# Performance work log

Measured on AMD Instinct MI355X. Metric: run time of the kernel, lower is better.

The kernel has to match this reference:

```python
import jax, jax.numpy as jnp
import numpy as np


def setup_inputs() -> dict:
    key = jax.random.key(0)
    k1, k2 = jax.random.split(key)
    B, C, H = 1024, 1000, 512  # batch, classes, hidden
    y = jax.random.normal(k1, (B, C), dtype=jnp.float32)
    w = jax.random.normal(k2, (C, H), dtype=jnp.float32)
    epsilon = jnp.ones((), dtype=jnp.float32)
    lipschitz = jnp.ones((), dtype=jnp.float32)
    return {"y": y, "w": w, "epsilon": epsilon, "lipschitz": lipschitz}


def reference(y, w, epsilon, lipschitz):
    # y: [B, C] logits; w: [C, H] final-layer weight
    kW = lipschitz * w.T                      # [H, C]
    j = jnp.argmax(y, axis=1)                 # [B]
    y_j = jnp.max(y, axis=1, keepdims=True)   # [B, 1]
    kW_j = kW.T[j]                            # [B, H] gather of argmax column
    kW_ij = kW_j[:, :, None] - kW[None]       # [B, H, C] broadcast difference
    sq = jnp.sum(kW_ij * kW_ij, axis=1)       # [B, C]
    # safe sqrt (value identical; avoids NaN grad at the exact-zero j column)
    K_ij = jnp.where(sq > 0, jnp.sqrt(jnp.where(sq > 0, sq, 1.0)), 0.0)
    y_bot_i = y + epsilon * K_ij              # [B, C]
    y_bot_i = jnp.where(y == y_j, -jnp.inf, y_bot_i)
    y_bot = jnp.max(y_bot_i, axis=1, keepdims=True)  # [B, 1]
    return jnp.concatenate([y, y_bot], axis=1)       # [B, C+1]
```

## Files before the change

### kernel.cpp

```cpp
#include <hip/hip_runtime.h>
#include <math.h>

#define B_SZ 1024
#define C_SZ 1000
#define H_SZ 512


typedef __attribute__((ext_vector_type(8))) short bf16x8;
typedef __attribute__((ext_vector_type(4))) float f32x4;

__global__ __launch_bounds__(256) void k_prep(
    const float* __restrict__ y, const float* __restrict__ w,
    int* __restrict__ jv, float* __restrict__ ymax,
    float* __restrict__ wnorm, short* __restrict__ wbf,
    float* __restrict__ out) {
    const int r = blockIdx.x;
    const int tid = threadIdx.x;
    if (r < 250) {
        const int wave = tid >> 6, lane = tid & 63;
        const int c = r * 4 + wave;
        const float* row = w + c * H_SZ;
        float4 a = *(const float4*)(row + lane * 8);
        float4 b = *(const float4*)(row + lane * 8 + 4);
        float f[8] = {a.x, a.y, a.z, a.w, b.x, b.y, b.z, b.w};
        unsigned short u[8];
        float s = 0.f;
#pragma unroll
        for (int i = 0; i < 8; ++i) {
            s += f[i] * f[i];
            unsigned v = __float_as_uint(f[i]);
            v += 0x7fffu + ((v >> 16) & 1u);
            u[i] = (unsigned short)(v >> 16);
        }
        uint4 pk;
        pk.x = (unsigned)u[0] | ((unsigned)u[1] << 16);
        pk.y = (unsigned)u[2] | ((unsigned)u[3] << 16);
        pk.z = (unsigned)u[4] | ((unsigned)u[5] << 16);
        pk.w = (unsigned)u[6] | ((unsigned)u[7] << 16);
        *(uint4*)(wbf + c * H_SZ + lane * 8) = pk;
#pragma unroll
        for (int off = 32; off; off >>= 1) s += __shfl_down(s, off, 64);
        if (lane == 0) wnorm[c] = s;
    } else {
        const int b = r - 250;
        const float* yrow = y + b * C_SZ;
        float* orow = out + b * (C_SZ + 1);
        float best = -INFINITY;
        int bidx = 0x7fffffff;
        if (tid < 250) {
            float4 v = *(const float4*)(yrow + tid * 4);
            float e[4] = {v.x, v.y, v.z, v.w};
#pragma unroll
            for (int i = 0; i < 4; ++i) {
                orow[tid * 4 + i] = e[i];
                if (e[i] > best) { best = e[i]; bidx = tid * 4 + i; }
            }
        }
        const int lane = tid & 63;
#pragma unroll
        for (int off = 32; off; off >>= 1) {
            float ov = __shfl_down(best, off, 64);
            int oi = __shfl_down(bidx, off, 64);
            if (ov > best || (ov == best && oi < bidx)) { best = ov; bidx = oi; }
        }
        __shared__ float sv[4];
        __shared__ int si[4];
        if (lane == 0) { sv[tid >> 6] = best; si[tid >> 6] = bidx; }
        __syncthreads();
        if (tid == 0) {
            float bv = sv[0]; int bi = si[0];
#pragma unroll
            for (int k = 1; k < 4; ++k) {
                if (sv[k] > bv || (sv[k] == bv && si[k] < bi)) { bv = sv[k]; bi = si[k]; }
            }
            jv[b] = bi;
            ymax[b] = bv;
        }
    }
}

#define KC 128
#define RS 136
__global__ __launch_bounds__(256) void k_main(
    const float* __restrict__ y, const short* __restrict__ wbf,
    const float* __restrict__ eps_p, const float* __restrict__ lip_p,
    const int* __restrict__ jv, const float* __restrict__ ymax,
    const float* __restrict__ wnorm, float* __restrict__ part) {
    __shared__ __align__(16) short As[64 * RS];
    __shared__ __align__(16) short Bs[64 * RS];
    __shared__ int sjv[64];
    __shared__ float snj[64];
    __shared__ float sym[64];

    const int t = threadIdx.x;
    const int bx = blockIdx.x, by = blockIdx.y;
    const int b0 = by * 64, c0 = bx * 64;

    if (t < 64) {
        int j = jv[b0 + t];
        sjv[t] = j;
        snj[t] = wnorm[j];
        sym[t] = ymax[b0 + t];
    }
    __syncthreads();

    const int srow = t >> 2;
    const int sseg = t & 3;
    int crow = c0 + srow; if (crow > C_SZ - 1) crow = C_SZ - 1;
    const short* agsrc = wbf + sjv[srow] * H_SZ;
    const short* bgsrc = wbf + crow * H_SZ;

    uint4 pa[4], pb[4];
#pragma unroll
    for (int p = 0; p < 4; ++p) {
        const int off = (sseg + p * 4) * 8;
        pa[p] = *(const uint4*)(agsrc + off);
        pb[p] = *(const uint4*)(bgsrc + off);
    }

    const int wv = t >> 6, lane = t & 63;
    const int col = lane & 15, quad = lane >> 4;
    const short* ard = &As[(wv * 16 + col) * RS + quad * 8];
    const short* brd = &Bs[col * RS + quad * 8];

    f32x4 acc[4] = {{0.f, 0.f, 0.f, 0.f},
                    {0.f, 0.f, 0.f, 0.f},
                    {0.f, 0.f, 0.f, 0.f},
                    {0.f, 0.f, 0.f, 0.f}};

    for (int ch = 0; ch < 4; ++ch) {
#pragma unroll
        for (int p = 0; p < 4; ++p) {
            const int off = (sseg + p * 4) * 8;
            *(uint4*)&As[srow * RS + off] = pa[p];
            *(uint4*)&Bs[srow * RS + off] = pb[p];
        }
        __syncthreads();
        if (ch < 3) {
            const int gbase = (ch + 1) * KC;
#pragma unroll
            for (int p = 0; p < 4; ++p) {
                const int off = gbase + (sseg + p * 4) * 8;
                pa[p] = *(const uint4*)(agsrc + off);
                pb[p] = *(const uint4*)(bgsrc + off);
            }
        }
#pragma unroll
        for (int ks = 0; ks < 4; ++ks) {
            bf16x8 af = *(const bf16x8*)(ard + ks * 32);
#pragma unroll
            for (int ct = 0; ct < 4; ++ct) {
                bf16x8 bf = *(const bf16x8*)(brd + ct * 16 * RS + ks * 32);
                acc[ct] =
                    __builtin_amdgcn_mfma_f32_16x16x32_bf16(af, bf, acc[ct], 0, 0, 0);
            }
        }
        __syncthreads();
    }

    const float eps = *eps_p;
    const float L = *lip_p;
    const float L2 = L * L;
    float rmax[4];
#pragma unroll
    for (int i = 0; i < 4; ++i) {
        const int br = wv * 16 + quad * 4 + i;
        const int b = b0 + br;
        const float nj = snj[br];
        const float ym = sym[br];
        float m = -INFINITY;
#pragma unroll
        for (int ct = 0; ct < 4; ++ct) {
            const int cc = c0 + ct * 16 + col;
            if (cc < C_SZ) {
                const float yv = y[b * C_SZ + cc];
                const float nc = wnorm[cc];
                const float sq = L2 * (nj + nc - 2.0f * acc[ct][i]);
                const float K = sq > 0.f ? sqrtf(sq) : 0.f;
                const float cand = (yv == ym) ? -INFINITY : yv + eps * K;
                m = fmaxf(m, cand);
            }
        }
        rmax[i] = m;
    }
#pragma unroll
    for (int off = 8; off; off >>= 1)
#pragma unroll
        for (int i = 0; i < 4; ++i)
            rmax[i] = fmaxf(rmax[i], __shfl_xor(rmax[i], off, 64));
    if (col == 0) {
        float* slice = part + bx * B_SZ;
#pragma unroll
        for (int i = 0; i < 4; ++i)
            slice[b0 + wv * 16 + quad * 4 + i] = rmax[i];
    }
}

__global__ void k_final(const float* __restrict__ part,
                        float* __restrict__ out) {
    int b = blockIdx.x * 256 + threadIdx.x;
    if (b >= B_SZ) return;
    float m = -INFINITY;
#pragma unroll
    for (int s = 0; s < 16; ++s) m = fmaxf(m, part[s * B_SZ + b]);
    out[b * (C_SZ + 1) + C_SZ] = m;
}

extern "C" void kernel_launch(void* const* d_in, const int* in_sizes, int n_in,
                              void* d_out, int out_size, void* d_ws,
                              size_t ws_size, hipStream_t stream) {
    const float* y = (const float*)d_in[0];
    const float* w = (const float*)d_in[1];
    const float* eps = (const float*)d_in[2];
    const float* lip = (const float*)d_in[3];
    float* out = (float*)d_out;

    char* ws = (char*)d_ws;
    int* jv = (int*)ws;
    float* ymax = (float*)(ws + 4096);
    float* wnorm = (float*)(ws + 8192);
    float* part = (float*)(ws + 16384);
    short* wbf = (short*)(ws + 524288);

    k_prep<<<250 + B_SZ, 256, 0, stream>>>(y, w, jv, ymax, wnorm, wbf, out);
    k_main<<<dim3(16, 16), 256, 0, stream>>>(y, wbf, eps, lip, jv, ymax, wnorm,
                                             part);
    k_final<<<(B_SZ + 255) / 256, 256, 0, stream>>>(part, out);
}
```

Baseline: 82.66 us.

## Fuse prep, main and final kernels into one cooperative kernel with grid syncs

Merges the three kernels into a single cooperative launch of 256 blocks. Each block handles weight conversion for some rows, does a per-wave argmax over four y rows, grid-syncs, runs the bf16 MFMA tile, grid-syncs again, and then reduces the partial maxima. The aim is to drop two launch gaps and the separate tiny final kernel. In exchange it adds grid-wide barrier overhead, and the prep phase now runs on fewer blocks with more work per wave.

Measured after the change: 138.0 us. 1.67x slower.

```diff
diff --git a/kernel.cpp b/kernel.cpp
--- a/kernel.cpp
+++ b/kernel.cpp
@@ -1,5 +1,8 @@
 #include <hip/hip_runtime.h>
+#include <hip/hip_cooperative_groups.h>
 #include <math.h>
+
+namespace cg = cooperative_groups;
 
 #define B_SZ 1024
 #define C_SZ 1000
@@ -9,16 +12,28 @@
 typedef __attribute__((ext_vector_type(8))) short bf16x8;
 typedef __attribute__((ext_vector_type(4))) float f32x4;
 
-__global__ __launch_bounds__(256) void k_prep(
+#define KC 128
+#define RS 136
+
+__global__ __launch_bounds__(256) void k_fused(
     const float* __restrict__ y, const float* __restrict__ w,
+    const float* __restrict__ eps_p, const float* __restrict__ lip_p,
     int* __restrict__ jv, float* __restrict__ ymax,
     float* __restrict__ wnorm, short* __restrict__ wbf,
-    float* __restrict__ out) {
+    float* __restrict__ part, float* __restrict__ out) {
+    __shared__ __align__(16) short As[64 * RS];
+    __shared__ __align__(16) short Bs[64 * RS];
+    __shared__ int sjv[64];
+    __shared__ float snj[64];
+    __shared__ float sym[64];
+
+    cg::grid_group grid = cg::this_grid();
     const int r = blockIdx.x;
-    const int tid = threadIdx.x;
+    const int t = threadIdx.x;
+    const int wv = t >> 6, lane = t & 63;
+
     if (r < 250) {
-        const int wave = tid >> 6, lane = tid & 63;
-        const int c = r * 4 + wave;
+        const int c = r * 4 + wv;
         const float* row = w + c * H_SZ;
         float4 a = *(const float4*)(row + lane * 8);
         float4 b = *(const float4*)(row + lane * 8 + 4);
@@ -41,59 +56,42 @@
 #pragma unroll
         for (int off = 32; off; off >>= 1) s += __shfl_down(s, off, 64);
         if (lane == 0) wnorm[c] = s;
-    } else {
-        const int b = r - 250;
+    }
+
+    {
+        const int b = r * 4 + wv;
         const float* yrow = y + b * C_SZ;
         float* orow = out + b * (C_SZ + 1);
         float best = -INFINITY;
         int bidx = 0x7fffffff;
-        if (tid < 250) {
-            float4 v = *(const float4*)(yrow + tid * 4);
-            float e[4] = {v.x, v.y, v.z, v.w};
-#pragma unroll
-            for (int i = 0; i < 4; ++i) {
-                orow[tid * 4 + i] = e[i];
-                if (e[i] > best) { best = e[i]; bidx = tid * 4 + i; }
-            }
-        }
-        const int lane = tid & 63;
+#pragma unroll
+        for (int i = 0; i < 4; ++i) {
+            const int idx = i * 64 + lane;
+            if (idx < 250) {
+                float4 v = *(const float4*)(yrow + idx * 4);
+                *(float4*)(orow + idx * 4) = v;
+                float e[4] = {v.x, v.y, v.z, v.w};
+#pragma unroll
+                for (int j = 0; j < 4; ++j) {
+                    if (e[j] > best) { best = e[j]; bidx = idx * 4 + j; }
+                }
+            }
+        }
 #pragma unroll
         for (int off = 32; off; off >>= 1) {
             float ov = __shfl_down(best, off, 64);
             int oi = __shfl_down(bidx, off, 64);
             if (ov > best || (ov == best && oi < bidx)) { best = ov; bidx = oi; }
         }
-        __shared__ float sv[4];
-        __shared__ int si[4];
-        if (lane == 0) { sv[tid >> 6] = best; si[tid >> 6] = bidx; }
-        __syncthreads();
-        if (tid == 0) {
-            float bv = sv[0]; int bi = si[0];
-#pragma unroll
-            for (int k = 1; k < 4; ++k) {
-                if (sv[k] > bv || (sv[k] == bv && si[k] < bi)) { bv = sv[k]; bi = si[k]; }
-            }
-            jv[b] = bi;
-            ymax[b] = bv;
-        }
-    }
-}
-
-#define KC 128
-#define RS 136
-__global__ __launch_bounds__(256) void k_main(
-    const float* __restrict__ y, const short* __restrict__ wbf,
-    const float* __restrict__ eps_p, const float* __restrict__ lip_p,
-    const int* __restrict__ jv, const float* __restrict__ ymax,
-    const float* __restrict__ wnorm, float* __restrict__ part) {
-    __shared__ __align__(16) short As[64 * RS];
-    __shared__ __align__(16) short Bs[64 * RS];
-    __shared__ int sjv[64];
-    __shared__ float snj[64];
-    __shared__ float sym[64];
-
-    const int t = threadIdx.x;
-    const int bx = blockIdx.x, by = blockIdx.y;
+        if (lane == 0) {
+            jv[b] = bidx;
+            ymax[b] = best;
+        }
+    }
+
+    grid.sync();
+
+    const int by = r >> 4, bx = r & 15;
     const int b0 = by * 64, c0 = bx * 64;
 
     if (t < 64) {
@@ -106,7 +104,8 @@
 
     const int srow = t >> 2;
     const int sseg = t & 3;
-    int crow = c0 + srow; if (crow > C_SZ - 1) crow = C_SZ - 1;
+    int crow = c0 + srow;
+    if (crow > C_SZ - 1) crow = C_SZ - 1;
     const short* agsrc = wbf + sjv[srow] * H_SZ;
     const short* bgsrc = wbf + crow * H_SZ;
 
@@ -118,7 +117,6 @@
         pb[p] = *(const uint4*)(bgsrc + off);
     }
 
-    const int wv = t >> 6, lane = t & 63;
     const int col = lane & 15, quad = lane >> 4;
     const short* ard = &As[(wv * 16 + col) * RS + quad * 8];
     const short* brd = &Bs[col * RS + quad * 8];
@@ -151,8 +149,8 @@
 #pragma unroll
             for (int ct = 0; ct < 4; ++ct) {
                 bf16x8 bf = *(const bf16x8*)(brd + ct * 16 * RS + ks * 32);
-                acc[ct] =
-                    __builtin_amdgcn_mfma_f32_16x16x32_bf16(af, bf, acc[ct], 0, 0, 0);
+                acc[ct] = __builtin_amdgcn_mfma_f32_16x16x32_bf16(af, bf,
+                                                                  acc[ct], 0, 0, 0);
             }
         }
         __syncthreads();
@@ -194,16 +192,18 @@
         for (int i = 0; i < 4; ++i)
             slice[b0 + wv * 16 + quad * 4 + i] = rmax[i];
     }
-}
-
-__global__ void k_final(const float* __restrict__ part,
-                        float* __restrict__ out) {
-    int b = blockIdx.x * 256 + threadIdx.x;
-    if (b >= B_SZ) return;
-    float m = -INFINITY;
-#pragma unroll
-    for (int s = 0; s < 16; ++s) m = fmaxf(m, part[s * B_SZ + b]);
-    out[b * (C_SZ + 1) + C_SZ] = m;
+
+    grid.sync();
+
+    {
+        const int rr = r * 4 + wv;
+        float m = -INFINITY;
+        if (lane < 16) m = part[lane * B_SZ + rr];
+#pragma unroll
+        for (int off = 8; off; off >>= 1)
+            m = fmaxf(m, __shfl_xor(m, off, 64));
+        if (lane == 0) out[rr * (C_SZ + 1) + C_SZ] = m;
+    }
 }
 
 extern "C" void kernel_launch(void* const* d_in, const int* in_sizes, int n_in,
@@ -222,8 +222,9 @@
     float* part = (float*)(ws + 16384);
     short* wbf = (short*)(ws + 524288);
 
-    k_prep<<<250 + B_SZ, 256, 0, stream>>>(y, w, jv, ymax, wnorm, wbf, out);
-    k_main<<<dim3(16, 16), 256, 0, stream>>>(y, wbf, eps, lip, jv, ymax, wnorm,
-                                             part);
-    k_final<<<(B_SZ + 255) / 256, 256, 0, stream>>>(part, out);
+    void* args[] = {(void*)&y,    (void*)&w,    (void*)&eps,  (void*)&lip,
+                    (void*)&jv,   (void*)&ymax, (void*)&wnorm, (void*)&wbf,
+                    (void*)&part, (void*)&out};
+    hipLaunchCooperativeKernel((void*)k_fused, dim3(256), dim3(256), args, 0,
+                               stream);
 }
```

## Shrink main-kernel batch tile to 16 rows to launch more blocks

Applied to the files above, without the earlier changes.

The main kernel's batch tile drops from 64 to 16 rows per block. Each wave now handles one 16x16 output tile with a single accumulator, and the grid grows from 256 to 1024 blocks to fill more compute units on the GPU. Per-block row maxima are combined across waves through shared memory before being written out. The cost is that each 64-row class tile of weights is reloaded four times as often, and each block does less work relative to its fixed overhead.

Measured after the change: 86.28 us. 1.04x slower.

```diff
diff --git a/kernel.cpp b/kernel.cpp
--- a/kernel.cpp
+++ b/kernel.cpp
@@ -8,6 +8,9 @@
 
 typedef __attribute__((ext_vector_type(8))) short bf16x8;
 typedef __attribute__((ext_vector_type(4))) float f32x4;
+
+#define KC 128
+#define RS 136
 
 __global__ __launch_bounds__(256) void k_prep(
     const float* __restrict__ y, const float* __restrict__ w,
@@ -79,24 +82,25 @@
     }
 }
 
-#define KC 128
-#define RS 136
 __global__ __launch_bounds__(256) void k_main(
     const float* __restrict__ y, const short* __restrict__ wbf,
     const float* __restrict__ eps_p, const float* __restrict__ lip_p,
     const int* __restrict__ jv, const float* __restrict__ ymax,
     const float* __restrict__ wnorm, float* __restrict__ part) {
-    __shared__ __align__(16) short As[64 * RS];
+    __shared__ __align__(16) short As[16 * RS];
     __shared__ __align__(16) short Bs[64 * RS];
-    __shared__ int sjv[64];
-    __shared__ float snj[64];
-    __shared__ float sym[64];
+    __shared__ int sjv[16];
+    __shared__ float snj[16];
+    __shared__ float sym[16];
+    __shared__ float wred[4][16];
 
     const int t = threadIdx.x;
+    const int wv = t >> 6, lane = t & 63;
+    const int col = lane & 15, quad = lane >> 4;
     const int bx = blockIdx.x, by = blockIdx.y;
-    const int b0 = by * 64, c0 = bx * 64;
-
-    if (t < 64) {
+    const int b0 = by * 16, c0 = bx * 64;
+
+    if (t < 16) {
         int j = jv[b0 + t];
         sjv[t] = j;
         snj[t] = wnorm[j];
@@ -104,56 +108,48 @@
     }
     __syncthreads();
 
-    const int srow = t >> 2;
-    const int sseg = t & 3;
-    int crow = c0 + srow; if (crow > C_SZ - 1) crow = C_SZ - 1;
-    const short* agsrc = wbf + sjv[srow] * H_SZ;
-    const short* bgsrc = wbf + crow * H_SZ;
-
-    uint4 pa[4], pb[4];
+    const int arow = t >> 4;
+    const int aseg = t & 15;
+    const short* ag = wbf + sjv[arow] * H_SZ + aseg * 8;
+    int browv[4], bsegv[4];
+    const short* bg[4];
 #pragma unroll
     for (int p = 0; p < 4; ++p) {
-        const int off = (sseg + p * 4) * 8;
-        pa[p] = *(const uint4*)(agsrc + off);
-        pb[p] = *(const uint4*)(bgsrc + off);
-    }
-
-    const int wv = t >> 6, lane = t & 63;
-    const int col = lane & 15, quad = lane >> 4;
-    const short* ard = &As[(wv * 16 + col) * RS + quad * 8];
-    const short* brd = &Bs[col * RS + quad * 8];
-
-    f32x4 acc[4] = {{0.f, 0.f, 0.f, 0.f},
-                    {0.f, 0.f, 0.f, 0.f},
-                    {0.f, 0.f, 0.f, 0.f},
-                    {0.f, 0.f, 0.f, 0.f}};
+        const int idx = p * 256 + t;
+        browv[p] = idx >> 4;
+        bsegv[p] = idx & 15;
+        int cr = c0 + browv[p];
+        if (cr > C_SZ - 1) cr = C_SZ - 1;
+        bg[p] = wbf + cr * H_SZ + bsegv[p] * 8;
+    }
+
+    uint4 pa = *(const uint4*)ag;
+    uint4 pb[4];
+#pragma unroll
+    for (int p = 0; p < 4; ++p) pb[p] = *(const uint4*)bg[p];
+
+    const short* ard = &As[col * RS + quad * 8];
+    const short* brd = &Bs[(wv * 16 + col) * RS + quad * 8];
+
+    f32x4 acc = {0.f, 0.f, 0.f, 0.f};
 
     for (int ch = 0; ch < 4; ++ch) {
-#pragma unroll
-        for (int p = 0; p < 4; ++p) {
-            const int off = (sseg + p * 4) * 8;
-            *(uint4*)&As[srow * RS + off] = pa[p];
-            *(uint4*)&Bs[srow * RS + off] = pb[p];
-        }
+        *(uint4*)&As[arow * RS + aseg * 8] = pa;
+#pragma unroll
+        for (int p = 0; p < 4; ++p)
+            *(uint4*)&Bs[browv[p] * RS + bsegv[p] * 8] = pb[p];
         __syncthreads();
         if (ch < 3) {
-            const int gbase = (ch + 1) * KC;
-#pragma unroll
-            for (int p = 0; p < 4; ++p) {
-                const int off = gbase + (sseg + p * 4) * 8;
-                pa[p] = *(const uint4*)(agsrc + off);
-                pb[p] = *(const uint4*)(bgsrc + off);
-            }
+            const int go = (ch + 1) * KC;
+            pa = *(const uint4*)(ag + go);
+#pragma unroll
+            for (int p = 0; p < 4; ++p) pb[p] = *(const uint4*)(bg[p] + go);
         }
 #pragma unroll
         for (int ks = 0; ks < 4; ++ks) {
             bf16x8 af = *(const bf16x8*)(ard + ks * 32);
-#pragma unroll
-            for (int ct = 0; ct < 4; ++ct) {
-                bf16x8 bf = *(const bf16x8*)(brd + ct * 16 * RS + ks * 32);
-                acc[ct] =
-                    __builtin_amdgcn_mfma_f32_16x16x32_bf16(af, bf, acc[ct], 0, 0, 0);
-            }
+            bf16x8 bf = *(const bf16x8*)(brd + ks * 32);
+            acc = __builtin_amdgcn_mfma_f32_16x16x32_bf16(af, bf, acc, 0, 0, 0);
         }
         __syncthreads();
     }
@@ -161,27 +157,21 @@
     const float eps = *eps_p;
     const float L = *lip_p;
     const float L2 = L * L;
+    const int cc = c0 + wv * 16 + col;
+    const float nc = wnorm[cc < C_SZ ? cc : C_SZ - 1];
     float rmax[4];
 #pragma unroll
     for (int i = 0; i < 4; ++i) {
-        const int br = wv * 16 + quad * 4 + i;
+        const int br = quad * 4 + i;
         const int b = b0 + br;
-        const float nj = snj[br];
-        const float ym = sym[br];
-        float m = -INFINITY;
-#pragma unroll
-        for (int ct = 0; ct < 4; ++ct) {
-            const int cc = c0 + ct * 16 + col;
-            if (cc < C_SZ) {
-                const float yv = y[b * C_SZ + cc];
-                const float nc = wnorm[cc];
-                const float sq = L2 * (nj + nc - 2.0f * acc[ct][i]);
-                const float K = sq > 0.f ? sqrtf(sq) : 0.f;
-                const float cand = (yv == ym) ? -INFINITY : yv + eps * K;
-                m = fmaxf(m, cand);
-            }
-        }
-        rmax[i] = m;
+        float cand = -INFINITY;
+        if (cc < C_SZ) {
+            const float yv = y[b * C_SZ + cc];
+            const float sq = L2 * (snj[br] + nc - 2.0f * acc[i]);
+            const float K = sq > 0.f ? sqrtf(sq) : 0.f;
+            cand = (yv == sym[br]) ? -INFINITY : yv + eps * K;
+        }
+        rmax[i] = cand;
     }
 #pragma unroll
     for (int off = 8; off; off >>= 1)
@@ -189,10 +179,14 @@
         for (int i = 0; i < 4; ++i)
             rmax[i] = fmaxf(rmax[i], __shfl_xor(rmax[i], off, 64));
     if (col == 0) {
-        float* slice = part + bx * B_SZ;
-#pragma unroll
-        for (int i = 0; i < 4; ++i)
-            slice[b0 + wv * 16 + quad * 4 + i] = rmax[i];
+#pragma unroll
+        for (int i = 0; i < 4; ++i) wred[wv][quad * 4 + i] = rmax[i];
+    }
+    __syncthreads();
+    if (t < 16) {
+        float m = fmaxf(fmaxf(wred[0][t], wred[1][t]),
+                        fmaxf(wred[2][t], wred[3][t]));
+        part[bx * B_SZ + b0 + t] = m;
     }
 }
 
@@ -223,7 +217,7 @@
     short* wbf = (short*)(ws + 524288);
 
     k_prep<<<250 + B_SZ, 256, 0, stream>>>(y, w, jv, ymax, wnorm, wbf, out);
-    k_main<<<dim3(16, 16), 256, 0, stream>>>(y, wbf, eps, lip, jv, ymax, wnorm,
+    k_main<<<dim3(16, 64), 256, 0, stream>>>(y, wbf, eps, lip, jv, ymax, wnorm,
                                              part);
     k_final<<<(B_SZ + 255) / 256, 256, 0, stream>>>(part, out);
 }
```
